# Kernel tuning notes

Hardware: AMD Instinct MI355X
Metric: run time of the kernel (lower is better)

Reference implementation:

```python
import jax, jax.numpy as jnp
import numpy as np

B, N, D = 16, 4096, 128
M = 2048  # codebook size
EPS = 1e-10


def setup_inputs() -> dict:
    key = jax.random.key(0)
    kx, kw = jax.random.split(key)
    x = jax.random.normal(kx, (B, N, D), dtype=jnp.float32)
    # codebook (nn.Embedding weight, kaiming-uniform init ~ uniform(-bound, bound))
    bound = np.sqrt(6.0 / D)
    weight = jax.random.uniform(kw, (M, D), dtype=jnp.float32, minval=-bound, maxval=bound)
    return {"x": x, "weight": weight}


def reference(x, weight):
    b, n, d = x.shape
    m = weight.shape[0]
    q = x.reshape(b * n, d)                       # (bn, d)
    # squared L2 distances: ||q||^2 + ||k||^2 - 2 q.k  (temperature==0 -> argmax of -dist)
    l2_q = jnp.sum(q * q, axis=1, keepdims=True)  # (bn, 1)
    l2_k = jnp.sum(weight * weight, axis=1)       # (m,)
    sim = q @ weight.T                            # (bn, m)  GEMM
    dist = l2_q + l2_k - 2.0 * sim
    indices = jnp.argmin(dist, axis=1)            # (bn,)
    z = weight[indices]                           # onehot @ k == gather
    quantized = z.reshape(b, n, d)
    # straight-through estimator (training path): q + (z - q).detach()
    quantized_st = x + jax.lax.stop_gradient(quantized - x)
    # commitment loss: mse(quantized.detach(), x)
    loss = jnp.mean((jax.lax.stop_gradient(quantized_st) - x) ** 2)
    # perplexity over codebook usage (h == 1 head)
    counts = jnp.zeros((m,), dtype=x.dtype).at[indices].add(1.0)
    p = counts / (b * n)                          # mean of onehot over (b, n)
    perp = jnp.exp(-jnp.sum(p * jnp.log(p + EPS)))[None]  # shape (1,) == 'h'
    out_indices = indices.reshape(b, 1, n)
    return quantized_st, loss, perp, out_indices
```

## Files before the change

kernel.cpp:

```cpp
#include <hip/hip_runtime.h>
#include <hip/hip_bf16.h>
#include <math.h>

#define D_DIM 128
#define M_CODES 2048
#define BN_TOT 65536
#define OUT_LOSS 8388608
#define OUT_PERP 8388609
#define OUT_IDX 8388610
#define MARGIN 2e-3f

#define QB 64

#define WS_L2K 0
#define WS_PB 8192
#define WS_IDX 1056768
#define WS_PART 1318912
#define WS_CNT 1351680
#define WS_FLAGCNT 1359872
#define WS_FLAGGED 1360896

typedef __bf16 bf16x8 __attribute__((ext_vector_type(8)));
typedef float f32x4 __attribute__((ext_vector_type(4)));

#define GLOAD_LDS16(g, l)                                         \
  __builtin_amdgcn_global_load_lds(                               \
      (const __attribute__((address_space(1))) void*)(g),         \
      (__attribute__((address_space(3))) void*)(l), 16, 0, 0)

#define MFMA16(a, b, c) __builtin_amdgcn_mfma_f32_16x16x32_bf16((a), (b), (c), 0, 0, 0)

__global__ __launch_bounds__(256) void l2_kernel(const float* __restrict__ w,
                                                 float* __restrict__ l2k) {
  int i = blockIdx.x * 256 + threadIdx.x;
  const float4* p = (const float4*)(w + (size_t)i * D_DIM);
  double s = 0.0;
#pragma unroll
  for (int j = 0; j < 32; ++j) {
    float4 v = p[j];
    s += (double)(v.x * v.x);
    s += (double)(v.y * v.y);
    s += (double)(v.z * v.z);
    s += (double)(v.w * v.w);
  }
  l2k[i] = (float)s;
}

__global__ __launch_bounds__(256) void pack_w_chunk(const float* __restrict__ w,
                                                    __bf16* __restrict__ pb) {
  int gid = blockIdx.x * 256 + threadIdx.x;
  int lane = gid & 63;
  int g = gid >> 6;
  int cid = g & 15;
  int ch = g >> 4;
  int k2 = cid & 7;
  int ks = k2 >> 1;
  int wc = k2 & 1;
  int code = ch * 32 + wc * 16 + (lane & 15);
  int koff = ks * 32 + (lane >> 4) * 8;
  const float* src = w + (size_t)code * D_DIM + koff;
  float4 u = *(const float4*)src;
  float4 v = *(const float4*)(src + 4);
  float f[8] = {u.x, u.y, u.z, u.w, v.x, v.y, v.z, v.w};
  bf16x8 o;
#pragma unroll
  for (int j = 0; j < 8; ++j) {
    __bf16 hh = (__bf16)f[j];
    o[j] = (cid < 8) ? hh : (__bf16)(f[j] - (float)hh);
  }
  *(bf16x8*)(pb + (size_t)g * 512 + lane * 8) = o;
}

__device__ __forceinline__ void merge_bs(float& b, float& s, int& i,
                                         float ob, float os, int oi) {
  if (ob > b) {
    s = fmaxf(b, os);
    b = ob;
    i = oi;
  } else if (ob < b) {
    s = fmaxf(s, ob);
  } else {
    s = b;
    if (oi < i) i = oi;
  }
}

__global__ __launch_bounds__(256, 4) void argmin_mfma(
    const float* __restrict__ x, const __bf16* __restrict__ pb,
    const float* __restrict__ l2k, int* __restrict__ best_idx,
    int* __restrict__ flag_count, int* __restrict__ flagged) {
  __shared__ __align__(16) unsigned char ldsB[2][16384];
  __shared__ float redB[4][32];
  __shared__ float redS[4][32];
  __shared__ int redI[4][32];

  const int tid = threadIdx.x;
  const int wv = tid >> 6;
  const int lane = tid & 63;
  const int col = lane & 15;
  const int quad = lane >> 4;
  const int wc = wv & 1;
  const int wq = wv >> 1;
  const int q0 = blockIdx.x * QB;

  bf16x8 ah[2][4], al[2][4];
#pragma unroll
  for (int mt = 0; mt < 2; ++mt) {
#pragma unroll
    for (int ks = 0; ks < 4; ++ks) {
      const float* xr =
          x + (size_t)(q0 + wq * 32 + 16 * mt + col) * D_DIM + 32 * ks + 8 * quad;
      float4 u = *(const float4*)xr;
      float4 v = *(const float4*)(xr + 4);
      float f[8] = {u.x, u.y, u.z, u.w, v.x, v.y, v.z, v.w};
      bf16x8 h, l;
#pragma unroll
      for (int j = 0; j < 8; ++j) {
        __bf16 hh = (__bf16)f[j];
        h[j] = hh;
        l[j] = (__bf16)(f[j] - (float)hh);
      }
      ah[mt][ks] = h;
      al[mt][ks] = l;
    }
  }

  float m1[2][4], m2[2][4];
  int bc[2][4];
#pragma unroll
  for (int mt = 0; mt < 2; ++mt)
#pragma unroll
    for (int r = 0; r < 4; ++r) {
      m1[mt][r] = -3.4e38f;
      m2[mt][r] = -3.4e38f;
      bc[mt][r] = 0;
    }

  const char* pbase = (const char*)pb + (size_t)(wv * 4) * 1024 + (size_t)lane * 16;
  const int ldsw = wc * 1024 + lane * 16;
  const float* l2p = l2k + wc * 16 + col;

  auto stage = [&](int ch, int buf) {
    const char* s = pbase + (size_t)ch * 16384;
    unsigned char* d = &ldsB[buf][(wv * 4) * 1024];
    GLOAD_LDS16(s, d);
    GLOAD_LDS16(s + 1024, d + 1024);
    GLOAD_LDS16(s + 2048, d + 2048);
    GLOAD_LDS16(s + 3072, d + 3072);
  };

  auto compute = [&](int ch, int buf, float l2v) {
    float ini = -0.5f * l2v;
    f32x4 acc[2];
    acc[0] = (f32x4){ini, ini, ini, ini};
    acc[1] = (f32x4){ini, ini, ini, ini};
#pragma unroll
    for (int ks = 0; ks < 4; ++ks) {
      const unsigned char* base = &ldsB[buf][ks * 2048 + ldsw];
      bf16x8 bh = *(const bf16x8*)(base);
      bf16x8 bl = *(const bf16x8*)(base + 8192);
#pragma unroll
      for (int mt = 0; mt < 2; ++mt) {
        acc[mt] = MFMA16(al[mt][ks], bh, acc[mt]);
        acc[mt] = MFMA16(ah[mt][ks], bl, acc[mt]);
        acc[mt] = MFMA16(ah[mt][ks], bh, acc[mt]);
      }
    }
#pragma unroll
    for (int mt = 0; mt < 2; ++mt) {
#pragma unroll
      for (int r = 0; r < 4; ++r) {
        float dd = acc[mt][r];
        bool gt = dd > m1[mt][r];
        m2[mt][r] = fmaxf(m2[mt][r], fminf(m1[mt][r], dd));
        bc[mt][r] = gt ? ch : bc[mt][r];
        m1[mt][r] = fmaxf(m1[mt][r], dd);
      }
    }
  };

  stage(0, 0);
  float l2n0 = l2p[0];
  float l2n1 = l2p[32];
  __syncthreads();

#pragma unroll 1
  for (int cc = 0; cc < 32; ++cc) {
    const int ch0 = cc * 2;
    float l2c0 = l2n0, l2c1 = l2n1;
    if (cc < 31) {
      l2n0 = l2p[(ch0 + 2) * 32];
      l2n1 = l2p[(ch0 + 3) * 32];
    }
    stage(ch0 + 1, 1);
    compute(ch0, 0, l2c0);
    __syncthreads();
    if (cc < 31) stage(ch0 + 2, 0);
    compute(ch0 + 1, 1, l2c1);
    __syncthreads();
  }

#pragma unroll
  for (int mt = 0; mt < 2; ++mt) {
#pragma unroll
    for (int r = 0; r < 4; ++r) {
      float b = m1[mt][r], s = m2[mt][r];
      int i = bc[mt][r] * 32 + wc * 16 + col;
#pragma unroll
      for (int m = 1; m < 16; m <<= 1) {
        float ob = __shfl_xor(b, m);
        float os = __shfl_xor(s, m);
        int oi = __shfl_xor(i, m);
        merge_bs(b, s, i, ob, os, oi);
      }
      if (col == 0) {
        int qloc = 16 * mt + 4 * quad + r;
        redB[wv][qloc] = b;
        redS[wv][qloc] = s;
        redI[wv][qloc] = i;
      }
    }
  }
  __syncthreads();

  if (tid < QB) {
    int wq2 = tid >> 5;
    int ql = tid & 31;
    float b = -3.4e38f, s = -3.4e38f;
    int i = 0x7fffffff;
    merge_bs(b, s, i, redB[wq2 * 2 + 0][ql], redS[wq2 * 2 + 0][ql], redI[wq2 * 2 + 0][ql]);
    merge_bs(b, s, i, redB[wq2 * 2 + 1][ql], redS[wq2 * 2 + 1][ql], redI[wq2 * 2 + 1][ql]);
    best_idx[q0 + tid] = i;
    if (2.0f * (b - s) < MARGIN) {
      int pos = atomicAdd(flag_count, 1);
      flagged[pos] = q0 + tid;
    }
  }
}

__global__ __launch_bounds__(256) void fixup_kernel(const float* __restrict__ x,
                                                    const float* __restrict__ w,
                                                    const float* __restrict__ l2k32,
                                                    const int* __restrict__ flagged,
                                                    const int* __restrict__ flag_count,
                                                    int* __restrict__ best_idx) {
  __shared__ float qs[D_DIM];
  __shared__ float l2q_sh;
  __shared__ float redD[256];
  __shared__ int redI[256];
  const int tid = threadIdx.x;
  const int n = *flag_count;
  for (int f = blockIdx.x; f < n; f += gridDim.x) {
    __syncthreads();
    int q = flagged[f];
    if (tid < D_DIM) qs[tid] = x[(size_t)q * D_DIM + tid];
    __syncthreads();
    if (tid == 0) {
      double s = 0.0;
      for (int d = 0; d < D_DIM; ++d) {
        float t = qs[d] * qs[d];
        s += (double)t;
      }
      l2q_sh = (float)s;
    }
    __syncthreads();
    const float l2q = l2q_sh;
    float bd = 3.4e38f;
    int bi = 0x7fffffff;
    for (int c = tid; c < M_CODES; c += 256) {
      const float4* wr = (const float4*)(w + (size_t)c * D_DIM);
      double s = 0.0;
#pragma unroll
      for (int j = 0; j < 32; ++j) {
        float4 v = wr[j];
        s = fma((double)qs[j * 4 + 0], (double)v.x, s);
        s = fma((double)qs[j * 4 + 1], (double)v.y, s);
        s = fma((double)qs[j * 4 + 2], (double)v.z, s);
        s = fma((double)qs[j * 4 + 3], (double)v.w, s);
      }
      float simf = (float)s;
      float S = l2q + l2k32[c];
      float T = 2.0f * simf;
      float dist = S - T;
      if (dist < bd) { bd = dist; bi = c; }
    }
    redD[tid] = bd;
    redI[tid] = bi;
    __syncthreads();
    for (int off = 128; off; off >>= 1) {
      if (tid < off) {
        float od = redD[tid + off];
        int oi = redI[tid + off];
        if (od < redD[tid] || (od == redD[tid] && oi < redI[tid])) {
          redD[tid] = od;
          redI[tid] = oi;
        }
      }
      __syncthreads();
    }
    if (tid == 0) best_idx[q] = redI[0];
  }
}

__global__ __launch_bounds__(256) void epilogue_kernel(const float* __restrict__ x,
                                                       const float* __restrict__ w,
                                                       const int* __restrict__ best_idx,
                                                       float* __restrict__ out,
                                                       float* __restrict__ part,
                                                       int* __restrict__ counts) {
  int gid = blockIdx.x * 256 + threadIdx.x;
  int q = gid >> 5;
  int d4 = gid & 31;
  int idx = best_idx[q];
  float4 xv = ((const float4*)x)[gid];
  float4 wv = ((const float4*)w)[(size_t)idx * 32 + d4];
  float4 o;
  float t0 = wv.x - xv.x; o.x = xv.x + t0; float e0 = o.x - xv.x;
  float t1 = wv.y - xv.y; o.y = xv.y + t1; float e1 = o.y - xv.y;
  float t2 = wv.z - xv.z; o.z = xv.z + t2; float e2 = o.z - xv.z;
  float t3 = wv.w - xv.w; o.w = xv.w + t3; float e3 = o.w - xv.w;
  float ls = e0 * e0 + e1 * e1 + e2 * e2 + e3 * e3;
  ((float4*)out)[gid] = o;

  for (int off = 32; off; off >>= 1) ls += __shfl_down(ls, off);
  __shared__ float red[4];
  if ((threadIdx.x & 63) == 0) red[threadIdx.x >> 6] = ls;
  __syncthreads();
  if (threadIdx.x == 0) part[blockIdx.x] = red[0] + red[1] + red[2] + red[3];

  if (d4 == 0) {
    out[OUT_IDX + q] = (float)idx;
    atomicAdd(&counts[idx], 1);
  }
}

__global__ __launch_bounds__(256) void finalize_kernel(const int* __restrict__ counts,
                                                       const float* __restrict__ part,
                                                       float* __restrict__ out) {
  int tid = threadIdx.x;
  float ls = 0.f;
  for (int i = tid; i < 8192; i += 256) ls += part[i];
  float es = 0.f;
  for (int i = tid; i < M_CODES; i += 256) {
    float p = (float)counts[i] * (1.0f / 65536.0f);
    es += p * logf(p + 1e-10f);
  }
  for (int off = 32; off; off >>= 1) {
    ls += __shfl_down(ls, off);
    es += __shfl_down(es, off);
  }
  __shared__ float redl[4], rede[4];
  if ((tid & 63) == 0) {
    redl[tid >> 6] = ls;
    rede[tid >> 6] = es;
  }
  __syncthreads();
  if (tid == 0) {
    out[OUT_LOSS] = (redl[0] + redl[1] + redl[2] + redl[3]) * (1.0f / 8388608.0f);
    out[OUT_PERP] = expf(-(rede[0] + rede[1] + rede[2] + rede[3]));
  }
}

extern "C" void kernel_launch(void* const* d_in, const int* in_sizes, int n_in,
                              void* d_out, int out_size, void* d_ws, size_t ws_size,
                              hipStream_t stream) {
  const float* x = (const float*)d_in[0];
  const float* w = (const float*)d_in[1];
  float* out = (float*)d_out;
  char* ws = (char*)d_ws;
  float* l2k = (float*)(ws + WS_L2K);
  __bf16* pb = (__bf16*)(ws + WS_PB);
  int* bidx = (int*)(ws + WS_IDX);
  float* part = (float*)(ws + WS_PART);
  int* counts = (int*)(ws + WS_CNT);
  int* flagcnt = (int*)(ws + WS_FLAGCNT);
  int* flagged = (int*)(ws + WS_FLAGGED);

  hipMemsetAsync(counts, 0, M_CODES * sizeof(int), stream);
  hipMemsetAsync(flagcnt, 0, sizeof(int), stream);
  l2_kernel<<<8, 256, 0, stream>>>(w, l2k);
  pack_w_chunk<<<256, 256, 0, stream>>>(w, pb);
  argmin_mfma<<<BN_TOT / QB, 256, 0, stream>>>(x, pb, l2k, bidx, flagcnt, flagged);
  fixup_kernel<<<256, 256, 0, stream>>>(x, w, l2k, flagged, flagcnt, bidx);
  epilogue_kernel<<<8192, 256, 0, stream>>>(x, w, bidx, out, part, counts);
  finalize_kernel<<<1, 256, 0, stream>>>(counts, part, out);
}
```

Measured before the change: 259.5 us.

## Triple-buffer codebook staging with vmcnt waits and raise MFMA wave priority

The kernel moves from a double-buffered LDS ring with two full __syncthreads per chunk pair to a three-slot ring. It waits with an explicit s_waitcnt vmcnt(4) and a single barrier per chunk, so the load of chunk ch+2 overlaps the compute of chunk ch. The MFMA section is wrapped in s_setprio(1)/s_setprio(0) to favour waves that are issuing matrix ops. The cost is 48KB of LDS per block, with launch bounds lowered from 4 to 3 blocks per CU, which reduces occupancy and latency hiding across waves.

```diff
diff --git a/kernel.cpp b/kernel.cpp
--- a/kernel.cpp
+++ b/kernel.cpp
@@ -85,11 +85,11 @@
   }
 }
 
-__global__ __launch_bounds__(256, 4) void argmin_mfma(
+__global__ __launch_bounds__(256, 3) void argmin_mfma(
     const float* __restrict__ x, const __bf16* __restrict__ pb,
     const float* __restrict__ l2k, int* __restrict__ best_idx,
     int* __restrict__ flag_count, int* __restrict__ flagged) {
-  __shared__ __align__(16) unsigned char ldsB[2][16384];
+  __shared__ __align__(16) unsigned char ldsB[3 * 16384];
   __shared__ float redB[4][32];
   __shared__ float redS[4][32];
   __shared__ int redI[4][32];
@@ -140,23 +140,24 @@
   const int ldsw = wc * 1024 + lane * 16;
   const float* l2p = l2k + wc * 16 + col;
 
-  auto stage = [&](int ch, int buf) {
+  auto stage = [&](int ch, int bufOff) {
     const char* s = pbase + (size_t)ch * 16384;
-    unsigned char* d = &ldsB[buf][(wv * 4) * 1024];
+    unsigned char* d = &ldsB[bufOff + wv * 4096];
     GLOAD_LDS16(s, d);
     GLOAD_LDS16(s + 1024, d + 1024);
     GLOAD_LDS16(s + 2048, d + 2048);
     GLOAD_LDS16(s + 3072, d + 3072);
   };
 
-  auto compute = [&](int ch, int buf, float l2v) {
+  auto compute = [&](int ch, int bufOff, float l2v) {
     float ini = -0.5f * l2v;
     f32x4 acc[2];
     acc[0] = (f32x4){ini, ini, ini, ini};
     acc[1] = (f32x4){ini, ini, ini, ini};
+    __builtin_amdgcn_s_setprio(1);
 #pragma unroll
     for (int ks = 0; ks < 4; ++ks) {
-      const unsigned char* base = &ldsB[buf][ks * 2048 + ldsw];
+      const unsigned char* base = &ldsB[bufOff + ks * 2048 + ldsw];
       bf16x8 bh = *(const bf16x8*)(base);
       bf16x8 bl = *(const bf16x8*)(base + 8192);
 #pragma unroll
@@ -166,6 +167,7 @@
         acc[mt] = MFMA16(ah[mt][ks], bh, acc[mt]);
       }
     }
+    __builtin_amdgcn_s_setprio(0);
 #pragma unroll
     for (int mt = 0; mt < 2; ++mt) {
 #pragma unroll
@@ -179,26 +181,26 @@
     }
   };
 
+  float l2cur = l2p[0];
   stage(0, 0);
-  float l2n0 = l2p[0];
-  float l2n1 = l2p[32];
-  __syncthreads();
+  stage(1, 16384);
+  int offC = 0;
+  int offS = 32768;
 
 #pragma unroll 1
-  for (int cc = 0; cc < 32; ++cc) {
-    const int ch0 = cc * 2;
-    float l2c0 = l2n0, l2c1 = l2n1;
-    if (cc < 31) {
-      l2n0 = l2p[(ch0 + 2) * 32];
-      l2n1 = l2p[(ch0 + 3) * 32];
-    }
-    stage(ch0 + 1, 1);
-    compute(ch0, 0, l2c0);
-    __syncthreads();
-    if (cc < 31) stage(ch0 + 2, 0);
-    compute(ch0 + 1, 1, l2c1);
-    __syncthreads();
-  }
+  for (int ch = 0; ch < 63; ++ch) {
+    asm volatile("s_waitcnt vmcnt(4)" ::: "memory");
+    __builtin_amdgcn_s_barrier();
+    float l2nxt = l2p[(ch + 1) * 32];
+    if (ch < 62) stage(ch + 2, offS);
+    compute(ch, offC, l2cur);
+    l2cur = l2nxt;
+    offC += 16384; if (offC == 49152) offC = 0;
+    offS += 16384; if (offS == 49152) offS = 0;
+  }
+  asm volatile("s_waitcnt vmcnt(0)" ::: "memory");
+  __builtin_amdgcn_s_barrier();
+  compute(63, offC, l2cur);
 
 #pragma unroll
   for (int mt = 0; mt < 2; ++mt) {
```

New measurement: 271.7 us. 4.7% more time.

## Double codebook chunk size per pipeline stage to halve barrier count

Applied to the files above, without the earlier changes.

Each loop iteration now stages 64 codes (two 32-code sub-tiles, 32KB) into LDS instead of 32, so each wave computes two N-subtiles per iteration. This halves the number of __syncthreads and loop iterations across the 2048-code sweep, and lets the two sub-tiles' MFMA chains interleave for more independent work. In exchange LDS use doubles to 64KB per block and launch bounds drop to 2 blocks per CU, which lowers occupancy and latency hiding.

```diff
diff --git a/kernel.cpp b/kernel.cpp
--- a/kernel.cpp
+++ b/kernel.cpp
@@ -52,11 +52,11 @@
   int lane = gid & 63;
   int g = gid >> 6;
   int cid = g & 15;
-  int ch = g >> 4;
+  int p = g >> 4;
   int k2 = cid & 7;
   int ks = k2 >> 1;
   int wc = k2 & 1;
-  int code = ch * 32 + wc * 16 + (lane & 15);
+  int code = p * 32 + wc * 16 + (lane & 15);
   int koff = ks * 32 + (lane >> 4) * 8;
   const float* src = w + (size_t)code * D_DIM + koff;
   float4 u = *(const float4*)src;
@@ -85,11 +85,11 @@
   }
 }
 
-__global__ __launch_bounds__(256, 4) void argmin_mfma(
+__global__ __launch_bounds__(256, 2) void argmin_mfma(
     const float* __restrict__ x, const __bf16* __restrict__ pb,
     const float* __restrict__ l2k, int* __restrict__ best_idx,
     int* __restrict__ flag_count, int* __restrict__ flagged) {
-  __shared__ __align__(16) unsigned char ldsB[2][16384];
+  __shared__ __align__(16) unsigned char ldsB[2][32768];
   __shared__ float redB[4][32];
   __shared__ float redS[4][32];
   __shared__ int redI[4][32];
@@ -126,77 +126,81 @@
   }
 
   float m1[2][4], m2[2][4];
-  int bc[2][4];
+  int bp[2][4];
 #pragma unroll
   for (int mt = 0; mt < 2; ++mt)
 #pragma unroll
     for (int r = 0; r < 4; ++r) {
       m1[mt][r] = -3.4e38f;
       m2[mt][r] = -3.4e38f;
-      bc[mt][r] = 0;
-    }
-
-  const char* pbase = (const char*)pb + (size_t)(wv * 4) * 1024 + (size_t)lane * 16;
+      bp[mt][r] = 0;
+    }
+
   const int ldsw = wc * 1024 + lane * 16;
   const float* l2p = l2k + wc * 16 + col;
 
   auto stage = [&](int ch, int buf) {
-    const char* s = pbase + (size_t)ch * 16384;
-    unsigned char* d = &ldsB[buf][(wv * 4) * 1024];
-    GLOAD_LDS16(s, d);
-    GLOAD_LDS16(s + 1024, d + 1024);
-    GLOAD_LDS16(s + 2048, d + 2048);
-    GLOAD_LDS16(s + 3072, d + 3072);
+    const char* s = (const char*)pb + (size_t)ch * 32768 + wv * 8192 + lane * 16;
+    unsigned char* d = &ldsB[buf][wv * 8192];
+#pragma unroll
+    for (int i = 0; i < 8; ++i) GLOAD_LDS16(s + i * 1024, d + i * 1024);
   };
 
-  auto compute = [&](int ch, int buf, float l2v) {
-    float ini = -0.5f * l2v;
-    f32x4 acc[2];
-    acc[0] = (f32x4){ini, ini, ini, ini};
-    acc[1] = (f32x4){ini, ini, ini, ini};
+  auto compute = [&](int ch, int buf, float l2a, float l2b) {
+    float ia = -0.5f * l2a, ib = -0.5f * l2b;
+    f32x4 acc[2][2];
+    acc[0][0] = (f32x4){ia, ia, ia, ia};
+    acc[1][0] = (f32x4){ia, ia, ia, ia};
+    acc[0][1] = (f32x4){ib, ib, ib, ib};
+    acc[1][1] = (f32x4){ib, ib, ib, ib};
 #pragma unroll
     for (int ks = 0; ks < 4; ++ks) {
-      const unsigned char* base = &ldsB[buf][ks * 2048 + ldsw];
-      bf16x8 bh = *(const bf16x8*)(base);
-      bf16x8 bl = *(const bf16x8*)(base + 8192);
+#pragma unroll
+      for (int nt = 0; nt < 2; ++nt) {
+        const unsigned char* base = &ldsB[buf][nt * 16384 + ks * 2048 + ldsw];
+        bf16x8 bh = *(const bf16x8*)(base);
+        bf16x8 bl = *(const bf16x8*)(base + 8192);
+#pragma unroll
+        for (int mt = 0; mt < 2; ++mt) {
+          acc[mt][nt] = MFMA16(al[mt][ks], bh, acc[mt][nt]);
+          acc[mt][nt] = MFMA16(ah[mt][ks], bl, acc[mt][nt]);
+          acc[mt][nt] = MFMA16(ah[mt][ks], bh, acc[mt][nt]);
+        }
+      }
+    }
+#pragma unroll
+    for (int nt = 0; nt < 2; ++nt) {
 #pragma unroll
       for (int mt = 0; mt < 2; ++mt) {
-        acc[mt] = MFMA16(al[mt][ks], bh, acc[mt]);
-        acc[mt] = MFMA16(ah[mt][ks], bl, acc[mt]);
-        acc[mt] = MFMA16(ah[mt][ks], bh, acc[mt]);
-      }
-    }
-#pragma unroll
-    for (int mt = 0; mt < 2; ++mt) {
-#pragma unroll
-      for (int r = 0; r < 4; ++r) {
-        float dd = acc[mt][r];
-        bool gt = dd > m1[mt][r];
-        m2[mt][r] = fmaxf(m2[mt][r], fminf(m1[mt][r], dd));
-        bc[mt][r] = gt ? ch : bc[mt][r];
-        m1[mt][r] = fmaxf(m1[mt][r], dd);
+#pragma unroll
+        for (int r = 0; r < 4; ++r) {
+          float dd = acc[mt][nt][r];
+          bool gt = dd > m1[mt][r];
+          m2[mt][r] = fmaxf(m2[mt][r], fminf(m1[mt][r], dd));
+          bp[mt][r] = gt ? (ch * 2 + nt) : bp[mt][r];
+          m1[mt][r] = fmaxf(m1[mt][r], dd);
+        }
       }
     }
   };
 
   stage(0, 0);
-  float l2n0 = l2p[0];
-  float l2n1 = l2p[32];
+  float l2a = l2p[0];
+  float l2b = l2p[32];
   __syncthreads();
 
 #pragma unroll 1
-  for (int cc = 0; cc < 32; ++cc) {
-    const int ch0 = cc * 2;
-    float l2c0 = l2n0, l2c1 = l2n1;
-    if (cc < 31) {
-      l2n0 = l2p[(ch0 + 2) * 32];
-      l2n1 = l2p[(ch0 + 3) * 32];
-    }
-    stage(ch0 + 1, 1);
-    compute(ch0, 0, l2c0);
-    __syncthreads();
-    if (cc < 31) stage(ch0 + 2, 0);
-    compute(ch0 + 1, 1, l2c1);
+  for (int ch = 0; ch < 32; ++ch) {
+    const int buf = ch & 1;
+    if (ch < 31) stage(ch + 1, buf ^ 1);
+    float l2na = 0.f, l2nb = 0.f;
+    if (ch < 31) {
+      l2na = l2p[(2 * ch + 2) * 32];
+      l2nb = l2p[(2 * ch + 3) * 32];
+    }
+    compute(ch, buf, l2a, l2b);
+    l2a = l2na;
+    l2b = l2nb;
     __syncthreads();
   }
 
@@ -205,7 +209,7 @@
 #pragma unroll
     for (int r = 0; r < 4; ++r) {
       float b = m1[mt][r], s = m2[mt][r];
-      int i = bc[mt][r] * 32 + wc * 16 + col;
+      int i = bp[mt][r] * 32 + wc * 16 + col;
 #pragma unroll
       for (int m = 1; m < 16; m <<= 1) {
         float ob = __shfl_xor(b, m);
```

Measured after the change: 254.3 us. 1.02x faster.
